# Performance work log

Measured on AMD Instinct MI355X. Metric: run time of the kernel, lower is better.

Reference implementation:

```python
import jax, jax.numpy as jnp
import numpy as np

N_QKV = 64
N_EMBED = 2048
B = 4
T = 2048  # must equal N_EMBED because the module's causal mask is n_embed x n_embed


def setup_inputs() -> dict:
    key = jax.random.key(0)
    ks = jax.random.split(key, 7)
    s = 1.0 / np.sqrt(N_EMBED)
    return {
        "x": jax.random.normal(ks[0], (B, T, N_EMBED), dtype=jnp.float32),
        "Wq": jax.random.normal(ks[1], (N_QKV, N_EMBED), dtype=jnp.float32) * s,
        "bq": jnp.zeros((N_QKV,), dtype=jnp.float32),
        "Wk": jax.random.normal(ks[2], (N_QKV, N_EMBED), dtype=jnp.float32) * s,
        "bk": jnp.zeros((N_QKV,), dtype=jnp.float32),
        "Wv": jax.random.normal(ks[3], (N_QKV, N_EMBED), dtype=jnp.float32) * s,
        "bv": jnp.zeros((N_QKV,), dtype=jnp.float32),
    }


def reference(x, Wq, bq, Wk, bk, Wv, bv):
    # Linear projections: torch nn.Linear computes x @ W.T + b
    q = jnp.einsum("bte,qe->btq", x, Wq) + bq  # [B, T, n_qkv]
    k = jnp.einsum("bte,qe->btq", x, Wk) + bk
    v = jnp.einsum("bte,qe->btq", x, Wv) + bv
    scale = 1.0 / jnp.sqrt(jnp.asarray(N_QKV, dtype=x.dtype))
    logits = jnp.einsum("btq,bsq->bts", q, k) * scale  # [B, T, T]
    # causal mask: upper triangle (strictly above diagonal) -> -inf
    causal = jnp.tril(jnp.ones((T, T), dtype=bool))
    logits = jnp.where(causal, logits, jnp.asarray(-jnp.inf, dtype=logits.dtype))
    probs = jax.nn.softmax(logits, axis=-1)
    return jnp.einsum("bts,bsq->btq", probs, v)  # [B, T, n_qkv]
```

## Files before the change

### kernel.cpp

```cpp
#include <hip/hip_runtime.h>
#include <hip/hip_bf16.h>

#define T_SEQ 2048
#define E_DIM 2048
#define D_HEAD 64
#define B_SZ 4
#define NROWS (B_SZ * T_SEQ)

typedef __attribute__((ext_vector_type(8))) short bf16x8;
typedef __attribute__((ext_vector_type(4))) float f32x4;
typedef __attribute__((ext_vector_type(4))) unsigned short u16x4;
typedef __attribute__((ext_vector_type(8))) unsigned short u16x8;

__device__ __forceinline__ unsigned short f2bf(float x) {
    __hip_bfloat16 h = __float2bfloat16(x);
    return *reinterpret_cast<unsigned short*>(&h);
}

__device__ __forceinline__ u16x8 cvt8(float4 a, float4 b) {
    u16x8 t;
    t[0] = f2bf(a.x); t[1] = f2bf(a.y); t[2] = f2bf(a.z); t[3] = f2bf(a.w);
    t[4] = f2bf(b.x); t[5] = f2bf(b.y); t[6] = f2bf(b.z); t[7] = f2bf(b.w);
    return t;
}

__device__ __forceinline__ u16x4 cvt4(float4 a) {
    u16x4 t;
    t[0] = f2bf(a.x); t[1] = f2bf(a.y); t[2] = f2bf(a.z); t[3] = f2bf(a.w);
    return t;
}

__device__ __forceinline__ bf16x8 ldfrag(const unsigned short* p) {
    u16x4 lo = *(const u16x4*)p;
    u16x4 hi = *(const u16x4*)(p + 16);
    bf16x8 f;
    #pragma unroll
    for (int j = 0; j < 4; ++j) { f[j] = (short)lo[j]; f[4 + j] = (short)hi[j]; }
    return f;
}

__device__ __forceinline__ void lds_fence_barrier() {
    asm volatile("s_waitcnt lgkmcnt(0)" ::: "memory");
    __builtin_amdgcn_s_barrier();
}

__global__ __launch_bounds__(256) void wcvt_kernel(
    const float* __restrict__ Wq, const float* __restrict__ Wk,
    const float* __restrict__ Wv, unsigned short* __restrict__ Wp)
{
    const int gid = blockIdx.x * 256 + threadIdx.x;
    const int l    = gid & 63;
    const int k32  = (gid >> 6) & 63;
    const int f    = gid >> 12;
    const int r    = l & 15;
    const int g    = l >> 4;
    const int n    = 16 * f + r;
    const int pj   = n >> 6;
    const int o    = n & 63;
    const float* __restrict__ src = (pj == 0) ? Wq : (pj == 1) ? Wk : Wv;
    const float* p = src + (size_t)o * E_DIM + k32 * 32 + g * 4;
    float4 a = *(const float4*)p;
    float4 b = *(const float4*)(p + 16);
    *(u16x8*)(Wp + (size_t)gid * 8) = cvt8(a, b);
}

__global__ __launch_bounds__(768) void proj_mfma_kernel(
    const float* __restrict__ x, const unsigned short* __restrict__ Wp,
    const float* __restrict__ bq, const float* __restrict__ bk,
    const float* __restrict__ bv,
    __hip_bfloat16* __restrict__ qb, __hip_bfloat16* __restrict__ kb,
    __hip_bfloat16* __restrict__ vb)
{
    __shared__ unsigned short xs[2][32 * 72];

    const int tid  = threadIdx.x;
    const int w    = tid >> 6;
    const int l    = tid & 63;
    const int r    = l & 15;
    const int g    = l >> 4;
    const int wm   = (w >= 6) ? 1 : 0;
    const int wf   = (w >= 6) ? (w - 6) : w;
    const int row0 = blockIdx.x * 32;

    const bool stager = tid < 512;
    const int srow = tid >> 4;
    const int sc4  = (tid & 15) * 4;
    const float* xptr = x + (size_t)(row0 + srow) * E_DIM + sc4;

    const unsigned short* wb = Wp + (size_t)l * 8;

    f32x4 acc[2];
    acc[0] = (f32x4){0.f, 0.f, 0.f, 0.f};
    acc[1] = (f32x4){0.f, 0.f, 0.f, 0.f};

    float4 x0, xw, xf1;
    if (stager) {
        x0  = *(const float4*)(xptr);
        xw  = *(const float4*)(xptr + 64);
        xf1 = *(const float4*)(xptr + 128);
    }
    bf16x8 bcur[2][2];
    #pragma unroll
    for (int kk = 0; kk < 2; ++kk)
        #pragma unroll
        for (int ff = 0; ff < 2; ++ff)
            bcur[kk][ff] = *(const bf16x8*)(wb + (size_t)((2 * wf + ff) * 64 + kk) * 512);
    if (stager) *(u16x4*)&xs[0][srow * 72 + sc4] = cvt4(x0);
    lds_fence_barrier();

    for (int t = 0; t < 32; ++t) {
        const int cur = t & 1;

        float4 xf0;
        if (t < 29 && stager) xf0 = *(const float4*)(xptr + (t + 3) * 64);
        bf16x8 bnx[2][2];
        if (t < 31) {
            #pragma unroll
            for (int kk = 0; kk < 2; ++kk)
                #pragma unroll
                for (int ff = 0; ff < 2; ++ff)
                    bnx[kk][ff] = *(const bf16x8*)(
                        wb + (size_t)((2 * wf + ff) * 64 + 2 * (t + 1) + kk) * 512);
        }

        bf16x8 af[2];
        #pragma unroll
        for (int kk = 0; kk < 2; ++kk)
            af[kk] = ldfrag(&xs[cur][(wm * 16 + r) * 72 + kk * 32 + 4 * g]);

        if (t < 31 && stager) *(u16x4*)&xs[cur ^ 1][srow * 72 + sc4] = cvt4(xw);

        #pragma unroll
        for (int kk = 0; kk < 2; ++kk)
            #pragma unroll
            for (int ff = 0; ff < 2; ++ff)
                acc[ff] = __builtin_amdgcn_mfma_f32_16x16x32_bf16(
                    af[kk], bcur[kk][ff], acc[ff], 0, 0, 0);

        lds_fence_barrier();

        xw = xf1; xf1 = xf0;
        #pragma unroll
        for (int kk = 0; kk < 2; ++kk)
            #pragma unroll
            for (int ff = 0; ff < 2; ++ff)
                bcur[kk][ff] = bnx[kk][ff];
    }

    #pragma unroll
    for (int ff = 0; ff < 2; ++ff) {
        const int f  = 2 * wf + ff;
        const int n  = 16 * f + r;
        const int pj = n >> 6;
        const int o  = n & 63;
        const float* bias = (pj == 0) ? bq : (pj == 1) ? bk : bv;
        __hip_bfloat16* dst = (pj == 0) ? qb : (pj == 1) ? kb : vb;
        const float scale = (pj == 0) ? 0.18033688011112042f : 1.0f;
        const float bv_ = bias[o];
        #pragma unroll
        for (int j = 0; j < 4; ++j) {
            const int row = row0 + wm * 16 + 4 * g + j;
            dst[(size_t)row * D_HEAD + o] =
                __float2bfloat16((acc[ff][j] + bv_) * scale);
        }
    }
}

#define LDK 72
#define LDV 68
#define LDP 68

__global__ __launch_bounds__(128) void attn_part_kernel(
    const __hip_bfloat16* __restrict__ qg, const __hip_bfloat16* __restrict__ kg,
    const __hip_bfloat16* __restrict__ vg, float* __restrict__ Op,
    float* __restrict__ Ml, int tpc, int nch)
{
    const int qt = blockIdx.x;
    const int ch = blockIdx.y;
    const int total64 = qt / 2 + 1;
    if (ch * tpc >= total64) return;

    __shared__ unsigned short Kl[64 * LDK];
    __shared__ unsigned short Vt[64 * LDV];
    __shared__ unsigned short Pl[2 * 16 * LDP];

    const int tid = threadIdx.x;
    const int w   = tid >> 6;
    const int l   = tid & 63;
    const int r   = l & 15;
    const int g   = l >> 4;
    const int q0  = qt * 32;
    const int b   = blockIdx.z;
    const size_t base = (size_t)b * T_SEQ;

    const unsigned short* qb16 = (const unsigned short*)qg;
    const unsigned short* kb16 = (const unsigned short*)kg;
    const unsigned short* vb16 = (const unsigned short*)vg;

    const unsigned short* qrow = qb16 + (base + q0 + 16 * w + r) * D_HEAD;
    bf16x8 qf[2];
    #pragma unroll
    for (int kk = 0; kk < 2; ++kk)
        qf[kk] = ldfrag(qrow + 32 * kk + 4 * g);

    f32x4 acc_o[4];
    #pragma unroll
    for (int dn = 0; dn < 4; ++dn) acc_o[dn] = (f32x4){0.f, 0.f, 0.f, 0.f};
    float m4[4] = {-1e30f, -1e30f, -1e30f, -1e30f};
    float l4[4] = {0.f, 0.f, 0.f, 0.f};

    unsigned short* pw = &Pl[w * 16 * LDP];
    const int ntiles = min(tpc, total64 - ch * tpc);
    const int y = tid & 15, z = tid >> 4;
    const int s0base = ch * tpc * 64;

    u16x8 kr[4];
    u16x4 va4[4], vb4[4];

    auto issue = [&](int s0) {
        #pragma unroll
        for (int i = 0; i < 4; ++i) {
            const int c = tid + i * 128;
            kr[i] = *(const u16x8*)(kb16 + (base + s0 + (c >> 3)) * D_HEAD + (c & 7) * 8);
        }
        #pragma unroll
        for (int m = 0; m < 4; ++m) {
            const int sl = 2 * (z + 8 * m);
            const int d0 = y * 4;
            va4[m] = *(const u16x4*)(vb16 + (base + s0 + sl) * D_HEAD + d0);
            vb4[m] = *(const u16x4*)(vb16 + (base + s0 + sl + 1) * D_HEAD + d0);
        }
    };

    issue(s0base);

    for (int it = 0; it < ntiles; ++it) {
        const int s0 = s0base + it * 64;

        __builtin_amdgcn_s_barrier();

        #pragma unroll
        for (int i = 0; i < 4; ++i) {
            const int c = tid + i * 128;
            *(u16x8*)(&Kl[(c >> 3) * LDK + (c & 7) * 8]) = kr[i];
        }
        #pragma unroll
        for (int m = 0; m < 4; ++m) {
            const int sl = 2 * (z + 8 * m);
            const int d0 = y * 4;
            #pragma unroll
            for (int i = 0; i < 4; ++i) {
                unsigned int pr = (unsigned int)(unsigned short)va4[m][i] |
                                  ((unsigned int)(unsigned short)vb4[m][i] << 16);
                *(unsigned int*)&Vt[(d0 + i) * LDV + sl] = pr;
            }
        }
        lds_fence_barrier();

        if (it + 1 < ntiles) issue(s0 + 64);

        f32x4 s_acc[4];
        #pragma unroll
        for (int nt = 0; nt < 4; ++nt) s_acc[nt] = (f32x4){0.f, 0.f, 0.f, 0.f};
        #pragma unroll
        for (int nt = 0; nt < 4; ++nt)
            #pragma unroll
            for (int kk = 0; kk < 2; ++kk) {
                bf16x8 bf = ldfrag(&Kl[(nt * 16 + r) * LDK + kk * 32 + 4 * g]);
                s_acc[nt] = __builtin_amdgcn_mfma_f32_16x16x32_bf16(qf[kk], bf, s_acc[nt], 0, 0, 0);
            }

        if (s0 + 64 > q0) {
            #pragma unroll
            for (int nt = 0; nt < 4; ++nt)
                #pragma unroll
                for (int j = 0; j < 4; ++j)
                    if (s0 + nt * 16 + r > q0 + 16 * w + 4 * g + j)
                        s_acc[nt][j] = -1e30f;
        }

        float tm[4];
        #pragma unroll
        for (int j = 0; j < 4; ++j)
            tm[j] = fmaxf(fmaxf(s_acc[0][j], s_acc[1][j]),
                          fmaxf(s_acc[2][j], s_acc[3][j]));
        #pragma unroll
        for (int mask = 1; mask < 16; mask <<= 1)
            #pragma unroll
            for (int j = 0; j < 4; ++j)
                tm[j] = fmaxf(tm[j], __shfl_xor(tm[j], mask));

        float p[4][4], rs[4];
        #pragma unroll
        for (int j = 0; j < 4; ++j) {
            const float mn = fmaxf(m4[j], tm[j]);
            const float sc = exp2f(m4[j] - mn);
            m4[j] = mn;
            rs[j] = 0.f;
            #pragma unroll
            for (int nt = 0; nt < 4; ++nt) {
                p[nt][j] = exp2f(s_acc[nt][j] - mn);
                rs[j] += p[nt][j];
            }
            l4[j] *= sc;
            acc_o[0][j] *= sc; acc_o[1][j] *= sc;
            acc_o[2][j] *= sc; acc_o[3][j] *= sc;
        }
        #pragma unroll
        for (int mask = 1; mask < 16; mask <<= 1)
            #pragma unroll
            for (int j = 0; j < 4; ++j)
                rs[j] += __shfl_xor(rs[j], mask);
        #pragma unroll
        for (int j = 0; j < 4; ++j) l4[j] += rs[j];

        #pragma unroll
        for (int nt = 0; nt < 4; ++nt)
            #pragma unroll
            for (int j = 0; j < 4; ++j)
                pw[(4 * g + j) * LDP + nt * 16 + r] = f2bf(p[nt][j]);

        bf16x8 pf[2];
        #pragma unroll
        for (int kk = 0; kk < 2; ++kk)
            pf[kk] = ldfrag(&pw[r * LDP + kk * 32 + 4 * g]);

        #pragma unroll
        for (int dn = 0; dn < 4; ++dn)
            #pragma unroll
            for (int kk = 0; kk < 2; ++kk) {
                bf16x8 vf = ldfrag(&Vt[(dn * 16 + r) * LDV + kk * 32 + 4 * g]);
                acc_o[dn] = __builtin_amdgcn_mfma_f32_16x16x32_bf16(pf[kk], vf, acc_o[dn], 0, 0, 0);
            }
    }

    const size_t pidx = ((size_t)(b * 64 + qt) * nch + ch);
    float* op = Op + pidx * 2048;
    #pragma unroll
    for (int j = 0; j < 4; ++j) {
        const int row = 16 * w + 4 * g + j;
        #pragma unroll
        for (int dn = 0; dn < 4; ++dn)
            op[row * 64 + dn * 16 + r] = acc_o[dn][j];
        if (r == 0) {
            Ml[pidx * 64 + row]      = m4[j];
            Ml[pidx * 64 + 32 + row] = l4[j];
        }
    }
}

__global__ __launch_bounds__(256) void attn_combine_kernel(
    const float* __restrict__ Op, const float* __restrict__ Ml,
    float* __restrict__ out, int tpc, int nch)
{
    const int qt = blockIdx.x;
    const int b  = blockIdx.y;
    const int total64 = qt / 2 + 1;
    const int nact = (total64 + tpc - 1) / tpc;
    const size_t pbase = (size_t)(b * 64 + qt) * nch;

    __shared__ float wgt[8][32];
    __shared__ float linv[32];

    const int tid = threadIdx.x;
    if (tid < 32) {
        float M = -1e30f;
        for (int c = 0; c < nact; ++c)
            M = fmaxf(M, Ml[(pbase + c) * 64 + tid]);
        float L = 0.f;
        for (int c = 0; c < nact; ++c) {
            float wv = exp2f(Ml[(pbase + c) * 64 + tid] - M);
            wgt[c][tid] = wv;
            L += wv * Ml[(pbase + c) * 64 + 32 + tid];
        }
        linv[tid] = 1.0f / L;
    }
    __syncthreads();

    const int d  = tid & 63;
    const int r0 = tid >> 6;
    for (int row = r0; row < 32; row += 4) {
        float a = 0.f;
        for (int c = 0; c < nact; ++c)
            a += wgt[c][row] * Op[(pbase + c) * 2048 + row * 64 + d];
        out[((size_t)b * T_SEQ + qt * 32 + row) * D_HEAD + d] = a * linv[row];
    }
}

extern "C" void kernel_launch(void* const* d_in, const int* in_sizes, int n_in,
                              void* d_out, int out_size, void* d_ws, size_t ws_size,
                              hipStream_t stream) {
    const float* x  = (const float*)d_in[0];
    const float* Wq = (const float*)d_in[1];
    const float* bq = (const float*)d_in[2];
    const float* Wk = (const float*)d_in[3];
    const float* bk = (const float*)d_in[4];
    const float* Wv = (const float*)d_in[5];
    const float* bv = (const float*)d_in[6];
    float* out = (float*)d_out;

    __hip_bfloat16* qb = (__hip_bfloat16*)d_ws;
    __hip_bfloat16* kb = qb + (size_t)NROWS * D_HEAD;
    __hip_bfloat16* vb = kb + (size_t)NROWS * D_HEAD;
    unsigned short* Wp = (unsigned short*)(vb + (size_t)NROWS * D_HEAD);
    float* Op = (float*)((char*)d_ws + (4u << 20));

    int nch = 8;
    while (nch > 1 &&
           (4u << 20) + (size_t)256 * nch * (2048 + 64) * 4 > ws_size)
        nch >>= 1;
    const int tpc = 32 / nch;
    float* Ml = Op + (size_t)256 * nch * 2048;

    wcvt_kernel<<<192, 256, 0, stream>>>(Wq, Wk, Wv, Wp);
    proj_mfma_kernel<<<NROWS / 32, 768, 0, stream>>>(x, Wp, bq, bk, bv, qb, kb, vb);
    attn_part_kernel<<<dim3(64, nch, B_SZ), 128, 0, stream>>>(qb, kb, vb, Op, Ml, tpc, nch);
    attn_combine_kernel<<<dim3(64, B_SZ), 256, 0, stream>>>(Op, Ml, out, tpc, nch);
}
```

Before: 69.79 us.

## Stage entire x row tile into LDS upfront and remove per-step barriers

The projection kernel now loads the block's full 32x2048 x tile into LDS once, converting it to bf16, instead of double-buffering 64-column slices with a barrier each step. The main K loop then runs without synchronisation and is unrolled by two with separate even/odd weight register sets for prefetch. This removes 32 block barriers and the staging pipeline. In exchange it needs about 131KB of LDS per block, which limits occupancy to one block per CU and serialises the global load before any MFMA work can start.

```diff
diff --git a/kernel.cpp b/kernel.cpp
--- a/kernel.cpp
+++ b/kernel.cpp
@@ -71,7 +71,7 @@
     __hip_bfloat16* __restrict__ qb, __hip_bfloat16* __restrict__ kb,
     __hip_bfloat16* __restrict__ vb)
 {
-    __shared__ unsigned short xs[2][32 * 72];
+    __shared__ unsigned short xs[32 * 2056];
 
     const int tid  = threadIdx.x;
     const int w    = tid >> 6;
@@ -82,69 +82,83 @@
     const int wf   = (w >= 6) ? (w - 6) : w;
     const int row0 = blockIdx.x * 32;
 
-    const bool stager = tid < 512;
-    const int srow = tid >> 4;
-    const int sc4  = (tid & 15) * 4;
-    const float* xptr = x + (size_t)(row0 + srow) * E_DIM + sc4;
+    const float* xb = x + (size_t)row0 * E_DIM;
+    #pragma unroll
+    for (int bb = 0; bb < 3; ++bb) {
+        float4 v[7];
+        #pragma unroll
+        for (int i = 0; i < 7; ++i) {
+            const int c = tid + (bb * 7 + i) * 768;
+            v[i] = *(const float4*)(xb + ((c >> 9) * E_DIM + (c & 511) * 4));
+        }
+        #pragma unroll
+        for (int i = 0; i < 7; ++i) {
+            const int c = tid + (bb * 7 + i) * 768;
+            *(u16x4*)&xs[(c >> 9) * 2056 + (c & 511) * 4] = cvt4(v[i]);
+        }
+    }
+    if (tid < 256) {
+        const int c = 16128 + tid;
+        float4 v = *(const float4*)(xb + ((c >> 9) * E_DIM + (c & 511) * 4));
+        *(u16x4*)&xs[(c >> 9) * 2056 + (c & 511) * 4] = cvt4(v);
+    }
+    lds_fence_barrier();
 
     const unsigned short* wb = Wp + (size_t)l * 8;
+    const unsigned short* arow = &xs[(wm * 16 + r) * 2056 + 4 * g];
 
     f32x4 acc[2];
     acc[0] = (f32x4){0.f, 0.f, 0.f, 0.f};
     acc[1] = (f32x4){0.f, 0.f, 0.f, 0.f};
 
-    float4 x0, xw, xf1;
-    if (stager) {
-        x0  = *(const float4*)(xptr);
-        xw  = *(const float4*)(xptr + 64);
-        xf1 = *(const float4*)(xptr + 128);
-    }
-    bf16x8 bcur[2][2];
+    bf16x8 bE[2][2], bO[2][2];
     #pragma unroll
     for (int kk = 0; kk < 2; ++kk)
         #pragma unroll
-        for (int ff = 0; ff < 2; ++ff)
-            bcur[kk][ff] = *(const bf16x8*)(wb + (size_t)((2 * wf + ff) * 64 + kk) * 512);
-    if (stager) *(u16x4*)&xs[0][srow * 72 + sc4] = cvt4(x0);
-    lds_fence_barrier();
-
-    for (int t = 0; t < 32; ++t) {
-        const int cur = t & 1;
-
-        float4 xf0;
-        if (t < 29 && stager) xf0 = *(const float4*)(xptr + (t + 3) * 64);
-        bf16x8 bnx[2][2];
-        if (t < 31) {
+        for (int ff = 0; ff < 2; ++ff) {
+            bE[kk][ff] = *(const bf16x8*)(wb + (size_t)((2 * wf + ff) * 64 + 0 + kk) * 512);
+            bO[kk][ff] = *(const bf16x8*)(wb + (size_t)((2 * wf + ff) * 64 + 2 + kk) * 512);
+        }
+
+    for (int tt = 0; tt < 16; ++tt) {
+        const int t0 = 2 * tt, t1 = 2 * tt + 1;
+
+        bf16x8 afE[2], afO[2];
+        #pragma unroll
+        for (int kk = 0; kk < 2; ++kk) {
+            afE[kk] = ldfrag(arow + t0 * 64 + kk * 32);
+            afO[kk] = ldfrag(arow + t1 * 64 + kk * 32);
+        }
+
+        #pragma unroll
+        for (int kk = 0; kk < 2; ++kk)
+            #pragma unroll
+            for (int ff = 0; ff < 2; ++ff)
+                acc[ff] = __builtin_amdgcn_mfma_f32_16x16x32_bf16(
+                    afE[kk], bE[kk][ff], acc[ff], 0, 0, 0);
+        if (t0 + 2 < 32) {
             #pragma unroll
             for (int kk = 0; kk < 2; ++kk)
                 #pragma unroll
                 for (int ff = 0; ff < 2; ++ff)
-                    bnx[kk][ff] = *(const bf16x8*)(
-                        wb + (size_t)((2 * wf + ff) * 64 + 2 * (t + 1) + kk) * 512);
-        }
-
-        bf16x8 af[2];
-        #pragma unroll
-        for (int kk = 0; kk < 2; ++kk)
-            af[kk] = ldfrag(&xs[cur][(wm * 16 + r) * 72 + kk * 32 + 4 * g]);
-
-        if (t < 31 && stager) *(u16x4*)&xs[cur ^ 1][srow * 72 + sc4] = cvt4(xw);
+                    bE[kk][ff] = *(const bf16x8*)(
+                        wb + (size_t)((2 * wf + ff) * 64 + 2 * (t0 + 2) + kk) * 512);
+        }
 
         #pragma unroll
         for (int kk = 0; kk < 2; ++kk)
             #pragma unroll
             for (int ff = 0; ff < 2; ++ff)
                 acc[ff] = __builtin_amdgcn_mfma_f32_16x16x32_bf16(
-                    af[kk], bcur[kk][ff], acc[ff], 0, 0, 0);
-
-        lds_fence_barrier();
-
-        xw = xf1; xf1 = xf0;
-        #pragma unroll
-        for (int kk = 0; kk < 2; ++kk)
-            #pragma unroll
-            for (int ff = 0; ff < 2; ++ff)
-                bcur[kk][ff] = bnx[kk][ff];
+                    afO[kk], bO[kk][ff], acc[ff], 0, 0, 0);
+        if (t1 + 2 < 32) {
+            #pragma unroll
+            for (int kk = 0; kk < 2; ++kk)
+                #pragma unroll
+                for (int ff = 0; ff < 2; ++ff)
+                    bO[kk][ff] = *(const bf16x8*)(
+                        wb + (size_t)((2 * wf + ff) * 64 + 2 * (t1 + 2) + kk) * 512);
+        }
     }
 
     #pragma unroll
```

Result: slower. 71.63 us (+2.6%).

## Stage x and weights into LDS via direct global-to-LDS loads in projection

Applied to the files above, without the earlier changes.

Rewrites the projection GEMM's data staging so that fp32 x tiles and bf16 weight fragments go straight from global memory into double-buffered LDS with global_load_lds. The XOR-swizzled x tile is converted to bf16 when each wave reads its fragments. The block shrinks from 12 to 8 waves, and each wave now computes 3 output fragments instead of 2. The goal is to cut register staging and the stager-thread conversion work, and to overlap loads with MFMA. In exchange the fp32 x tile doubles LDS traffic, and every wave repeats the conversion.

```diff
diff --git a/kernel.cpp b/kernel.cpp
--- a/kernel.cpp
+++ b/kernel.cpp
@@ -24,10 +24,14 @@
     return t;
 }
 
-__device__ __forceinline__ u16x4 cvt4(float4 a) {
-    u16x4 t;
-    t[0] = f2bf(a.x); t[1] = f2bf(a.y); t[2] = f2bf(a.z); t[3] = f2bf(a.w);
-    return t;
+__device__ __forceinline__ bf16x8 cvtfrag2(f32x4 lo, f32x4 hi) {
+    bf16x8 f;
+    #pragma unroll
+    for (int j = 0; j < 4; ++j) {
+        f[j]     = (short)f2bf(lo[j]);
+        f[4 + j] = (short)f2bf(hi[j]);
+    }
+    return f;
 }
 
 __device__ __forceinline__ bf16x8 ldfrag(const unsigned short* p) {
@@ -42,6 +46,13 @@
 __device__ __forceinline__ void lds_fence_barrier() {
     asm volatile("s_waitcnt lgkmcnt(0)" ::: "memory");
     __builtin_amdgcn_s_barrier();
+}
+
+__device__ __forceinline__ void gl_lds16(const void* gsrc, void* ldst) {
+    __builtin_amdgcn_global_load_lds(
+        (const __attribute__((address_space(1))) unsigned int*)(unsigned long long)gsrc,
+        (__attribute__((address_space(3))) unsigned int*)(unsigned long long)ldst,
+        16, 0, 0);
 }
 
 __global__ __launch_bounds__(256) void wcvt_kernel(
@@ -64,92 +75,88 @@
     *(u16x8*)(Wp + (size_t)gid * 8) = cvt8(a, b);
 }
 
-__global__ __launch_bounds__(768) void proj_mfma_kernel(
+__global__ __launch_bounds__(512) void proj_mfma_kernel(
     const float* __restrict__ x, const unsigned short* __restrict__ Wp,
     const float* __restrict__ bq, const float* __restrict__ bk,
     const float* __restrict__ bv,
     __hip_bfloat16* __restrict__ qb, __hip_bfloat16* __restrict__ kb,
     __hip_bfloat16* __restrict__ vb)
 {
-    __shared__ unsigned short xs[2][32 * 72];
+    __shared__ unsigned char lds[2][32768];
 
     const int tid  = threadIdx.x;
     const int w    = tid >> 6;
     const int l    = tid & 63;
     const int r    = l & 15;
     const int g    = l >> 4;
-    const int wm   = (w >= 6) ? 1 : 0;
-    const int wf   = (w >= 6) ? (w - 6) : w;
+    const int wm   = w >> 2;
+    const int wn   = w & 3;
     const int row0 = blockIdx.x * 32;
 
-    const bool stager = tid < 512;
-    const int srow = tid >> 4;
-    const int sc4  = (tid & 15) * 4;
-    const float* xptr = x + (size_t)(row0 + srow) * E_DIM + sc4;
-
-    const unsigned short* wb = Wp + (size_t)l * 8;
-
-    f32x4 acc[2];
-    acc[0] = (f32x4){0.f, 0.f, 0.f, 0.f};
-    acc[1] = (f32x4){0.f, 0.f, 0.f, 0.f};
-
-    float4 x0, xw, xf1;
-    if (stager) {
-        x0  = *(const float4*)(xptr);
-        xw  = *(const float4*)(xptr + 64);
-        xf1 = *(const float4*)(xptr + 128);
-    }
-    bf16x8 bcur[2][2];
-    #pragma unroll
-    for (int kk = 0; kk < 2; ++kk)
-        #pragma unroll
-        for (int ff = 0; ff < 2; ++ff)
-            bcur[kk][ff] = *(const bf16x8*)(wb + (size_t)((2 * wf + ff) * 64 + kk) * 512);
-    if (stager) *(u16x4*)&xs[0][srow * 72 + sc4] = cvt4(x0);
-    lds_fence_barrier();
+    const int xrow = tid >> 4;
+    const int xjl  = (tid & 15) ^ (xrow & 7);
+    const unsigned char* xsrc =
+        (const unsigned char*)(x + (size_t)(row0 + xrow) * E_DIM + xjl * 4);
+    const int xdst = tid * 16;
+    const unsigned char* wsrc[3];
+    int wdst[3];
+    #pragma unroll
+    for (int i = 0; i < 3; ++i) {
+        const int cw = tid + i * 512;
+        const int f  = cw >> 7;
+        const int kc = (cw >> 6) & 1;
+        const int lw = cw & 63;
+        wsrc[i] = (const unsigned char*)Wp + (size_t)(f * 64 + kc) * 1024 + lw * 16;
+        wdst[i] = 8192 + cw * 16;
+    }
+
+    f32x4 acc[3];
+    #pragma unroll
+    for (int ff = 0; ff < 3; ++ff) acc[ff] = (f32x4){0.f, 0.f, 0.f, 0.f};
+
+    auto stage = [&](int t, int bi) {
+        gl_lds16(xsrc + (size_t)t * 256, &lds[bi][xdst]);
+        #pragma unroll
+        for (int i = 0; i < 3; ++i)
+            gl_lds16(wsrc[i] + (size_t)t * 2048, &lds[bi][wdst[i]]);
+    };
+
+    stage(0, 0);
+    asm volatile("s_waitcnt vmcnt(0)" ::: "memory");
+    __builtin_amdgcn_s_barrier();
+
+    const int arow  = wm * 16 + r;
+    const int amask = arow & 7;
+    const int abase = arow * 256;
 
     for (int t = 0; t < 32; ++t) {
         const int cur = t & 1;
-
-        float4 xf0;
-        if (t < 29 && stager) xf0 = *(const float4*)(xptr + (t + 3) * 64);
-        bf16x8 bnx[2][2];
-        if (t < 31) {
-            #pragma unroll
-            for (int kk = 0; kk < 2; ++kk)
-                #pragma unroll
-                for (int ff = 0; ff < 2; ++ff)
-                    bnx[kk][ff] = *(const bf16x8*)(
-                        wb + (size_t)((2 * wf + ff) * 64 + 2 * (t + 1) + kk) * 512);
-        }
+        if (t < 31) stage(t + 1, cur ^ 1);
 
         bf16x8 af[2];
         #pragma unroll
-        for (int kk = 0; kk < 2; ++kk)
-            af[kk] = ldfrag(&xs[cur][(wm * 16 + r) * 72 + kk * 32 + 4 * g]);
-
-        if (t < 31 && stager) *(u16x4*)&xs[cur ^ 1][srow * 72 + sc4] = cvt4(xw);
-
-        #pragma unroll
-        for (int kk = 0; kk < 2; ++kk)
-            #pragma unroll
-            for (int ff = 0; ff < 2; ++ff)
-                acc[ff] = __builtin_amdgcn_mfma_f32_16x16x32_bf16(
-                    af[kk], bcur[kk][ff], acc[ff], 0, 0, 0);
-
-        lds_fence_barrier();
-
-        xw = xf1; xf1 = xf0;
-        #pragma unroll
-        for (int kk = 0; kk < 2; ++kk)
-            #pragma unroll
-            for (int ff = 0; ff < 2; ++ff)
-                bcur[kk][ff] = bnx[kk][ff];
-    }
-
-    #pragma unroll
-    for (int ff = 0; ff < 2; ++ff) {
-        const int f  = 2 * wf + ff;
+        for (int kk = 0; kk < 2; ++kk) {
+            f32x4 lo = *(const f32x4*)&lds[cur][abase + (((kk * 8 + g)     ^ amask) * 16)];
+            f32x4 hi = *(const f32x4*)&lds[cur][abase + (((kk * 8 + 4 + g) ^ amask) * 16)];
+            af[kk] = cvtfrag2(lo, hi);
+        }
+        #pragma unroll
+        for (int ff = 0; ff < 3; ++ff) {
+            const int f = wn * 3 + ff;
+            #pragma unroll
+            for (int kk = 0; kk < 2; ++kk) {
+                bf16x8 bfm = *(const bf16x8*)&lds[cur][8192 + ((f * 2 + kk) * 64 + l) * 16];
+                acc[ff] = __builtin_amdgcn_mfma_f32_16x16x32_bf16(af[kk], bfm, acc[ff], 0, 0, 0);
+            }
+        }
+
+        asm volatile("s_waitcnt vmcnt(0)" ::: "memory");
+        __builtin_amdgcn_s_barrier();
+    }
+
+    #pragma unroll
+    for (int ff = 0; ff < 3; ++ff) {
+        const int f  = wn * 3 + ff;
         const int n  = 16 * f + r;
         const int pj = n >> 6;
         const int o  = n & 63;
@@ -413,7 +420,7 @@
     float* Ml = Op + (size_t)256 * nch * 2048;
 
     wcvt_kernel<<<192, 256, 0, stream>>>(Wq, Wk, Wv, Wp);
-    proj_mfma_kernel<<<NROWS / 32, 768, 0, stream>>>(x, Wp, bq, bk, bv, qb, kb, vb);
+    proj_mfma_kernel<<<NROWS / 32, 512, 0, stream>>>(x, Wp, bq, bk, bv, qb, kb, vb);
     attn_part_kernel<<<dim3(64, nch, B_SZ), 128, 0, stream>>>(qb, kb, vb, Op, Ml, tpc, nch);
     attn_combine_kernel<<<dim3(64, B_SZ), 256, 0, stream>>>(Op, Ml, out, tpc, nch);
 }
```

Result: slower. 71.35 us (+2.2%).
